# Optimization experiments

Measured on AMD Instinct MI355X. Metric: run time of the kernel, lower is better.

## Reference

```python
import jax, jax.numpy as jnp
import numpy as np

NG, NU, NI, H = 5000, 100000, 20000, 128
E_UG, E_UI, E_GI = 300000, 600000, 200000


def setup_inputs() -> dict:
    key = jax.random.key(0)
    ks = jax.random.split(key, 20)
    s = 0.05  # weight scale for numeric stability
    inp = {
        'x_group': jnp.arange(NG, dtype=jnp.int64) if False else jnp.arange(NG),
        'x_user': jnp.arange(NU),
        'x_item': jnp.arange(NI),
        'emb_group': jax.random.normal(ks[0], (NG, H), jnp.float32) * s,
        'emb_user': jax.random.normal(ks[1], (NU, H), jnp.float32) * s,
        'emb_item': jax.random.normal(ks[2], (NI, H), jnp.float32) * s,
        'W1l': jax.random.normal(ks[3], (6, H, H), jnp.float32) * s,
        'W1r': jax.random.normal(ks[4], (6, H, H), jnp.float32) * s,
        'b1': jax.random.normal(ks[5], (6, H), jnp.float32) * s,
        'W2l': jax.random.normal(ks[6], (6, H, H), jnp.float32) * s,
        'W2r': jax.random.normal(ks[7], (6, H, H), jnp.float32) * s,
        'b2': jax.random.normal(ks[8], (6, H), jnp.float32) * s,
        'pred_W': jax.random.normal(ks[9], (H, NI), jnp.float32) * s,
        'pred_b': jax.random.normal(ks[10], (NI,), jnp.float32) * s,
        'ug_src': jax.random.randint(ks[11], (E_UG,), 0, NU),
        'ug_dst': jax.random.randint(ks[12], (E_UG,), 0, NG),
        'ui_src': jax.random.randint(ks[13], (E_UI,), 0, NU),
        'ui_dst': jax.random.randint(ks[14], (E_UI,), 0, NI),
        'gi_src': jax.random.randint(ks[15], (E_GI,), 0, NG),
        'gi_dst': jax.random.randint(ks[16], (E_GI,), 0, NI),
    }
    return inp


def _seg_mean(x, src, dst, n_dst):
    # gather neighbor features [E, H], scatter-sum to dst, divide by in-degree
    s = jax.ops.segment_sum(x[src], dst, num_segments=n_dst)
    cnt = jax.ops.segment_sum(jnp.ones(dst.shape[0], x.dtype), dst, num_segments=n_dst)
    return s / jnp.clip(cnt, 1.0)[:, None]


def _hetero_sage_layer(hg, hu, hi, Wl, Wr, b,
                       ug_src, ug_dst, ui_src, ui_dst, gi_src, gi_dst):
    # edge-type order: 0 u2g, 1 g2u, 2 u2i, 3 i2u, 4 g2i, 5 i2g
    ng, nu, ni = hg.shape[0], hu.shape[0], hi.shape[0]
    og = (_seg_mean(hu, ug_src, ug_dst, ng) @ Wl[0] + hg @ Wr[0] + b[0]
          + _seg_mean(hi, gi_dst, gi_src, ng) @ Wl[5] + hg @ Wr[5] + b[5])
    ou = (_seg_mean(hg, ug_dst, ug_src, nu) @ Wl[1] + hu @ Wr[1] + b[1]
          + _seg_mean(hi, ui_dst, ui_src, nu) @ Wl[3] + hu @ Wr[3] + b[3])
    oi = (_seg_mean(hu, ui_src, ui_dst, ni) @ Wl[2] + hi @ Wr[2] + b[2]
          + _seg_mean(hg, gi_src, gi_dst, ni) @ Wl[4] + hi @ Wr[4] + b[4])
    return og, ou, oi


def reference(x_group, x_user, x_item, emb_group, emb_user, emb_item,
              W1l, W1r, b1, W2l, W2r, b2, pred_W, pred_b,
              ug_src, ug_dst, ui_src, ui_dst, gi_src, gi_dst):
    # embedding lookup; group embeddings are zeroed in BaseGR.forward
    hg = emb_group[x_group] * 0.0
    hu = emb_user[x_user]
    hi = emb_item[x_item]
    og, ou, oi = _hetero_sage_layer(hg, hu, hi, W1l, W1r, b1,
                                    ug_src, ug_dst, ui_src, ui_dst, gi_src, gi_dst)
    hg, hu, hi = jax.nn.relu(og), jax.nn.relu(ou), jax.nn.relu(oi)
    og, ou, oi = _hetero_sage_layer(hg, hu, hi, W2l, W2r, b2,
                                    ug_src, ug_dst, ui_src, ui_dst, gi_src, gi_dst)
    rep_group = jax.nn.relu(og)
    # eval-mode output: group-level item scores [NG, NI]
    return rep_group @ pred_W + pred_b
```

## Files before the change

kernel.cpp:

```cpp
#include <hip/hip_runtime.h>

typedef __bf16 bf16x8 __attribute__((ext_vector_type(8)));
typedef __bf16 bf16x4 __attribute__((ext_vector_type(4)));
typedef __bf16 bf16x2 __attribute__((ext_vector_type(2)));
typedef float  f32x4  __attribute__((ext_vector_type(4)));

#define NG 5000
#define NU 100000
#define NI 20000
#define H  128
#define EUG 300000
#define EUI 600000
#define EGI 200000
#define ETOT (EUG + EGI + EUI + EUI)
#define NN  (2 * NG + NU + NI)

#define B_EMBU  0UL
#define B_EMBI  25600000UL
#define B_AGGU  30720000UL
#define B_AGGI  56320000UL
#define B_AGGG1 61440000UL
#define B_AGGG2 62720000UL
#define B_HG1   64000000UL
#define B_GU    65280000UL
#define B_GI    66560000UL
#define B_REP   67840000UL
#define B_BC    69120000UL
#define B_PWT   69122048UL
#define B_WT    74242048UL
#define B_CNT   74536960UL
#define B_OFFS  75056960UL
#define B_CUR   75576976UL
#define B_EIDX  76096976UL



#define SCAN_CHUNK 2048
#define NCHUNK 64

__device__ __forceinline__ int swz(int row, int k) {
  return ((((k >> 3) ^ (row & 15)) << 3) | (k & 7));
}
__device__ __forceinline__ int cswz(int row, int col) {
  return col ^ (((row >> 2) & 1) << 4);
}

__global__ void prep_weights(const float* __restrict__ W1l, const float* __restrict__ W1r,
                             const float* __restrict__ W2l, const float* __restrict__ W2r,
                             const float* __restrict__ b1, const float* __restrict__ b2,
                             __bf16* __restrict__ WT, float* __restrict__ bc) {
  int b = blockIdx.x, tid = threadIdx.x;
  if (b < 9) {
    const float* Wa; const float* Wb = nullptr;
    switch (b) {
      case 0: Wa = W1r + 1 * 16384; Wb = W1r + 3 * 16384; break;
      case 1: Wa = W1l + 3 * 16384; break;
      case 2: Wa = W1l + 2 * 16384; break;
      case 3: Wa = W1r + 2 * 16384; Wb = W1r + 4 * 16384; break;
      case 4: Wa = W1l + 0 * 16384; break;
      case 5: Wa = W1l + 5 * 16384; break;
      case 6: Wa = W2r + 0 * 16384; Wb = W2r + 5 * 16384; break;
      case 7: Wa = W2l + 0 * 16384; break;
      default: Wa = W2l + 5 * 16384; break;
    }
    __bf16* dst = WT + b * 16384;
    for (int idx = tid; idx < 16384; idx += 256) {
      int k = idx >> 7, c = idx & 127;
      float v = Wa[idx];
      if (Wb) v += Wb[idx];
      dst[c * 128 + k] = (__bf16)v;
    }
  } else {
    if (tid < 128) {
      bc[tid]       = b1[128 + tid]     + b1[3 * 128 + tid];
      bc[128 + tid] = b1[2 * 128 + tid] + b1[4 * 128 + tid];
      bc[256 + tid] = b1[tid]           + b1[5 * 128 + tid];
      bc[384 + tid] = b2[tid]           + b2[5 * 128 + tid];
    }
  }
}

__global__ void transpose_predw(const float* __restrict__ pw, __bf16* __restrict__ pwt) {
  __shared__ float t[64][65];
  int i0 = blockIdx.x * 64, k0 = blockIdx.y * 64;
  int tid = threadIdx.x;
  for (int idx = tid; idx < 64 * 16; idx += 256) {
    int kk = idx >> 4, c4 = (idx & 15) << 2;
    int ib = i0 + c4;
    float x0 = 0.f, x1 = 0.f, x2 = 0.f, x3 = 0.f;
    const float* src = pw + (size_t)(k0 + kk) * NI + ib;
    if (ib + 3 < NI) {
      const float4 v = *(const float4*)src;
      x0 = v.x; x1 = v.y; x2 = v.z; x3 = v.w;
    } else {
      if (ib + 0 < NI) x0 = src[0];
      if (ib + 1 < NI) x1 = src[1];
      if (ib + 2 < NI) x2 = src[2];
      if (ib + 3 < NI) x3 = src[3];
    }
    t[kk][c4 + 0] = x0; t[kk][c4 + 1] = x1; t[kk][c4 + 2] = x2; t[kk][c4 + 3] = x3;
  }
  __syncthreads();
  for (int idx = tid; idx < 64 * 16; idx += 256) {
    int ii = idx >> 4, k4 = (idx & 15) << 2;
    int gi = i0 + ii;
    if (gi < NI) {
      bf16x4 o;
      o[0] = (__bf16)t[k4 + 0][ii]; o[1] = (__bf16)t[k4 + 1][ii];
      o[2] = (__bf16)t[k4 + 2][ii]; o[3] = (__bf16)t[k4 + 3][ii];
      *(bf16x4*)(pwt + (size_t)gi * 128 + k0 + k4) = o;
    }
  }
}

__global__ void cvt_bf16(const float* __restrict__ src, __bf16* __restrict__ dst, int n4) {
  int i = blockIdx.x * 256 + threadIdx.x;
  if (i < n4) {
    float4 v = ((const float4*)src)[i];
    bf16x4 o;
    o[0] = (__bf16)v.x; o[1] = (__bf16)v.y; o[2] = (__bf16)v.z; o[3] = (__bf16)v.w;
    ((bf16x4*)dst)[i] = o;
  }
}

__global__ void hist_all(const int* __restrict__ ug_dst, const int* __restrict__ gi_src,
                         const int* __restrict__ ui_src, const int* __restrict__ ui_dst,
                         int* __restrict__ cnt) {
  int i = blockIdx.x * 256 + threadIdx.x;
  int key, base;
  if (i < EUG)                       { key = ug_dst[i];                   base = 0; }
  else if (i < EUG + EGI)            { key = gi_src[i - EUG];             base = NG; }
  else if (i < EUG + EGI + EUI)      { key = ui_src[i - EUG - EGI];       base = 2 * NG; }
  else if (i < ETOT)                 { key = ui_dst[i - EUG - EGI - EUI]; base = 2 * NG + NU; }
  else return;
  atomicAdd(&cnt[base + key], 1);
}

__global__ void scan_k1(const int* __restrict__ cnt, int* __restrict__ chunksum) {
  __shared__ int ws[4];
  int b = blockIdx.x, tid = threadIdx.x, lane = tid & 63, w = tid >> 6;
  int base = b * SCAN_CHUNK + tid * 8;
  int s = 0;
#pragma unroll
  for (int j = 0; j < 8; ++j) { int i = base + j; if (i < NN) s += cnt[i]; }
#pragma unroll
  for (int d = 1; d < 64; d <<= 1) s += __shfl_xor(s, d, 64);
  if (lane == 0) ws[w] = s;
  __syncthreads();
  if (tid == 0) chunksum[b] = ws[0] + ws[1] + ws[2] + ws[3];
}

__global__ void scan_k2(const int* __restrict__ chunksum, int* __restrict__ chunkbase) {
  int lane = threadIdx.x;
  int v = chunksum[lane];
  int incl = v;
#pragma unroll
  for (int d = 1; d < 64; d <<= 1) { int t = __shfl_up(incl, d, 64); if (lane >= d) incl += t; }
  chunkbase[lane] = incl - v;
}

__global__ void scan_k3(const int* __restrict__ cnt, const int* __restrict__ chunkbase,
                        int* __restrict__ offs, int* __restrict__ cur) {
  __shared__ int ws[4];
  int b = blockIdx.x, tid = threadIdx.x, lane = tid & 63, w = tid >> 6;
  int base = b * SCAN_CHUNK + tid * 8;
  int x[8]; int s = 0;
#pragma unroll
  for (int j = 0; j < 8; ++j) { int i = base + j; x[j] = (i < NN) ? cnt[i] : 0; s += x[j]; }
  int incl = s;
#pragma unroll
  for (int d = 1; d < 64; d <<= 1) { int t = __shfl_up(incl, d, 64); if (lane >= d) incl += t; }
  if (lane == 63) ws[w] = incl;
  __syncthreads();
  int wpre = 0;
  for (int ww = 0; ww < w; ++ww) wpre += ws[ww];
  int excl = chunkbase[b] + wpre + incl - s;
#pragma unroll
  for (int j = 0; j < 8; ++j) {
    int i = base + j;
    if (i < NN) { offs[i] = excl; cur[i] = excl; }
    excl += x[j];
    if (i == NN - 1) offs[NN] = excl;
  }
}

__global__ void fill_all(const int* __restrict__ ug_src, const int* __restrict__ ug_dst,
                         const int* __restrict__ gi_src, const int* __restrict__ gi_dst,
                         const int* __restrict__ ui_src, const int* __restrict__ ui_dst,
                         int* __restrict__ cur, int* __restrict__ eidx) {
  int i = blockIdx.x * 256 + threadIdx.x;
  int key, base, payload;
  if (i < EUG)                  { key = ug_dst[i];       base = 0;            payload = ug_src[i]; }
  else if (i < EUG + EGI)       { int j = i - EUG;       key = gi_src[j]; base = NG;          payload = gi_dst[j]; }
  else if (i < EUG + EGI + EUI) { int j = i - EUG - EGI; key = ui_src[j]; base = 2 * NG;      payload = ui_dst[j]; }
  else if (i < ETOT)            { int j = i - EUG - EGI - EUI; key = ui_dst[j]; base = 2 * NG + NU; payload = ui_src[j]; }
  else return;
  int pos = atomicAdd(&cur[base + key], 1);
  eidx[pos] = payload;
}

__global__ __launch_bounds__(256)
void seg_mean_bf(const __bf16* __restrict__ feat, const int* __restrict__ offs,
                 const int* __restrict__ eidx, __bf16* __restrict__ out, int nnode) {
  int w = threadIdx.x >> 6, lane = threadIdx.x & 63;
  int node = blockIdx.x * 4 + w;
  if (node >= nnode) return;
  int s = offs[node], e = offs[node + 1];
  float a0 = 0.f, a1 = 0.f;
  int j = s;
  for (; j + 4 <= e; j += 4) {
    int i0 = eidx[j], i1 = eidx[j + 1], i2 = eidx[j + 2], i3 = eidx[j + 3];
    bf16x2 v0 = *(const bf16x2*)(feat + (size_t)i0 * 128 + lane * 2);
    bf16x2 v1 = *(const bf16x2*)(feat + (size_t)i1 * 128 + lane * 2);
    bf16x2 v2 = *(const bf16x2*)(feat + (size_t)i2 * 128 + lane * 2);
    bf16x2 v3 = *(const bf16x2*)(feat + (size_t)i3 * 128 + lane * 2);
    a0 += (float)v0[0] + (float)v1[0] + (float)v2[0] + (float)v3[0];
    a1 += (float)v0[1] + (float)v1[1] + (float)v2[1] + (float)v3[1];
  }
  for (; j < e; ++j) {
    int i0 = eidx[j];
    bf16x2 v0 = *(const bf16x2*)(feat + (size_t)i0 * 128 + lane * 2);
    a0 += (float)v0[0]; a1 += (float)v0[1];
  }
  float inv = (e > s) ? (1.f / (float)(e - s)) : 0.f;
  bf16x2 o;
  o[0] = (__bf16)(a0 * inv); o[1] = (__bf16)(a1 * inv);
  *(bf16x2*)(out + (size_t)node * 128 + lane * 2) = o;
}

__global__ __launch_bounds__(256)
void gemm_fused(const __bf16* __restrict__ A0, const __bf16* __restrict__ B0,
                const __bf16* __restrict__ A1, const __bf16* __restrict__ B1,
                const __bf16* __restrict__ A2, const __bf16* __restrict__ B2,
                const float* __restrict__ bias, float* __restrict__ Cf,
                __bf16* __restrict__ Cb, int N, int NC, int nterms, int relu) {
  __shared__ char smem_raw[128 * 128 * 4];
  __bf16* sA = (__bf16*)smem_raw;
  __bf16* sB = sA + 128 * 128;
  float* sC = (float*)smem_raw;
  int tid = threadIdx.x;
  int rowbase = blockIdx.x * 128, colbase = blockIdx.y * 128;
  int wid = tid >> 6, lane = tid & 63;
  int qrow = (wid >> 1) << 6, qcol = (wid & 1) << 6;
  int lrow = lane & 15, quad = lane >> 4;

  f32x4 acc[4][4];
#pragma unroll
  for (int mi = 0; mi < 4; ++mi)
#pragma unroll
    for (int ni = 0; ni < 4; ++ni) acc[mi][ni] = (f32x4){0.f, 0.f, 0.f, 0.f};

  const __bf16* As[3] = {A0, A1, A2};
  const __bf16* Bs[3] = {B0, B1, B2};

  for (int t = 0; t < nterms; ++t) {
    __syncthreads();
    const __bf16* A = As[t];
    for (int idx = tid; idx < 2048; idx += 256) {
      int row = idx >> 4, c8 = (idx & 15) << 3;
      int grow = rowbase + row;
      bf16x8 v;
      if (grow < N) v = *(const bf16x8*)(A + (size_t)grow * 128 + c8);
      else { for (int u = 0; u < 8; ++u) v[u] = (__bf16)0.f; }
      *(bf16x8*)&sA[row * 128 + swz(row, c8)] = v;
    }
    const __bf16* B = Bs[t];
    for (int idx = tid; idx < 2048; idx += 256) {
      int n = idx >> 4, c8 = (idx & 15) << 3;
      int gcol = colbase + n;
      bf16x8 v;
      if (gcol < NC) v = *(const bf16x8*)(B + (size_t)gcol * 128 + c8);
      else { for (int u = 0; u < 8; ++u) v[u] = (__bf16)0.f; }
      *(bf16x8*)&sB[n * 128 + swz(n, c8)] = v;
    }
    __syncthreads();
#pragma unroll
    for (int kb = 0; kb < 4; ++kb) {
      int k0 = kb * 32 + quad * 8;
      bf16x8 af[4], bfr[4];
#pragma unroll
      for (int mi = 0; mi < 4; ++mi) {
        int r = qrow + mi * 16 + lrow;
        af[mi] = *(const bf16x8*)&sA[r * 128 + swz(r, k0)];
      }
#pragma unroll
      for (int ni = 0; ni < 4; ++ni) {
        int r = qcol + ni * 16 + lrow;
        bfr[ni] = *(const bf16x8*)&sB[r * 128 + swz(r, k0)];
      }
#pragma unroll
      for (int mi = 0; mi < 4; ++mi)
#pragma unroll
        for (int ni = 0; ni < 4; ++ni)
          acc[mi][ni] = __builtin_amdgcn_mfma_f32_16x16x32_bf16(af[mi], bfr[ni], acc[mi][ni], 0, 0, 0);
    }
  }

  __syncthreads();
#pragma unroll
  for (int mi = 0; mi < 4; ++mi) {
#pragma unroll
    for (int ni = 0; ni < 4; ++ni) {
      int col = qcol + ni * 16 + lrow;
#pragma unroll
      for (int r = 0; r < 4; ++r) {
        int row = qrow + mi * 16 + quad * 4 + r;
        sC[row * 128 + cswz(row, col)] = acc[mi][ni][r];
      }
    }
  }
  __syncthreads();
  for (int idx = tid; idx < 4096; idx += 256) {
    int row = idx >> 5, c4 = (idx & 31) << 2;
    int grow = rowbase + row, gcol = colbase + c4;
    if (grow >= N) continue;
    f32x4 v = *(const f32x4*)&sC[row * 128 + cswz(row, c4)];
    if (gcol + 3 < NC) {
      f32x4 bv = *(const f32x4*)&bias[gcol];
      v += bv;
      if (relu) {
#pragma unroll
        for (int u = 0; u < 4; ++u) v[u] = fmaxf(v[u], 0.f);
      }
      if (Cb) {
        bf16x4 o;
        o[0] = (__bf16)v[0]; o[1] = (__bf16)v[1]; o[2] = (__bf16)v[2]; o[3] = (__bf16)v[3];
        *(bf16x4*)(Cb + (size_t)grow * NC + gcol) = o;
      } else {
        *(f32x4*)(Cf + (size_t)grow * NC + gcol) = v;
      }
    } else {
#pragma unroll
      for (int u = 0; u < 4; ++u) {
        if (gcol + u < NC) {
          float x = v[u] + bias[gcol + u];
          if (relu) x = fmaxf(x, 0.f);
          if (Cb) Cb[(size_t)grow * NC + gcol + u] = (__bf16)x;
          else    Cf[(size_t)grow * NC + gcol + u] = x;
        }
      }
    }
  }
}

extern "C" void kernel_launch(void* const* d_in, const int* in_sizes, int n_in,
                              void* d_out, int out_size, void* d_ws, size_t ws_size,
                              hipStream_t stream) {
  const float* emb_user = (const float*)d_in[4];
  const float* emb_item = (const float*)d_in[5];
  const float* W1l = (const float*)d_in[6];
  const float* W1r = (const float*)d_in[7];
  const float* b1  = (const float*)d_in[8];
  const float* W2l = (const float*)d_in[9];
  const float* W2r = (const float*)d_in[10];
  const float* b2  = (const float*)d_in[11];
  const float* predW = (const float*)d_in[12];
  const float* predb = (const float*)d_in[13];
  const int* ug_src = (const int*)d_in[14];
  const int* ug_dst = (const int*)d_in[15];
  const int* ui_src = (const int*)d_in[16];
  const int* ui_dst = (const int*)d_in[17];
  const int* gi_src = (const int*)d_in[18];
  const int* gi_dst = (const int*)d_in[19];

  char* ws = (char*)d_ws;
  __bf16* embU = (__bf16*)(ws + B_EMBU);
  __bf16* embI = (__bf16*)(ws + B_EMBI);
  __bf16* aggU = (__bf16*)(ws + B_AGGU);
  __bf16* aggI = (__bf16*)(ws + B_AGGI);
  __bf16* aggG1 = (__bf16*)(ws + B_AGGG1);
  __bf16* aggG2 = (__bf16*)(ws + B_AGGG2);
  __bf16* hg1 = (__bf16*)(ws + B_HG1);
  __bf16* gU  = (__bf16*)(ws + B_GU);
  __bf16* gI  = (__bf16*)(ws + B_GI);
  __bf16* rep = (__bf16*)(ws + B_REP);
  float* bc    = (float*)(ws + B_BC);
  __bf16* predWT = (__bf16*)(ws + B_PWT);
  __bf16* WT     = (__bf16*)(ws + B_WT);
  int* cnt  = (int*)(ws + B_CNT);
  int* offs = (int*)(ws + B_OFFS);
  int* cur  = (int*)(ws + B_CUR);
  int* eidx = (int*)(ws + B_EIDX);
  int* chunksum  = (int*)(ws + B_AGGU);
  int* chunkbase = chunksum + NCHUNK;

  const int* offs_ug  = offs;
  const int* offs_gi  = offs + NG;
  const int* offs_uiu = offs + 2 * NG;
  const int* offs_uii = offs + 2 * NG + NU;

  hipMemsetAsync(cnt, 0, NN * sizeof(int), stream);

  prep_weights<<<10, 256, 0, stream>>>(W1l, W1r, W2l, W2r, b1, b2, WT, bc);
  transpose_predw<<<dim3((NI + 63) / 64, 2), 256, 0, stream>>>(predW, predWT);
  cvt_bf16<<<(NU * 32 + 255) / 256, 256, 0, stream>>>(emb_user, embU, NU * 32);
  cvt_bf16<<<(NI * 32 + 255) / 256, 256, 0, stream>>>(emb_item, embI, NI * 32);

  hist_all<<<(ETOT + 255) / 256, 256, 0, stream>>>(ug_dst, gi_src, ui_src, ui_dst, cnt);
  scan_k1<<<NCHUNK, 256, 0, stream>>>(cnt, chunksum);
  scan_k2<<<1, 64, 0, stream>>>(chunksum, chunkbase);
  scan_k3<<<NCHUNK, 256, 0, stream>>>(cnt, chunkbase, offs, cur);
  fill_all<<<(ETOT + 255) / 256, 256, 0, stream>>>(ug_src, ug_dst, gi_src, gi_dst,
                                                   ui_src, ui_dst, cur, eidx);

  seg_mean_bf<<<(NU + 3) / 4, 256, 0, stream>>>(embI, offs_uiu, eidx, aggU, NU);
  seg_mean_bf<<<(NI + 3) / 4, 256, 0, stream>>>(embU, offs_uii, eidx, aggI, NI);
  seg_mean_bf<<<(NG + 3) / 4, 256, 0, stream>>>(embU, offs_ug, eidx, aggG1, NG);
  seg_mean_bf<<<(NG + 3) / 4, 256, 0, stream>>>(embI, offs_gi, eidx, aggG2, NG);

  gemm_fused<<<dim3((NU + 127) / 128, 1), 256, 0, stream>>>(
      embU, WT + 0 * 16384, aggU, WT + 1 * 16384, nullptr, nullptr,
      bc + 0, nullptr, aggU, NU, 128, 2, 1);
  gemm_fused<<<dim3((NI + 127) / 128, 1), 256, 0, stream>>>(
      aggI, WT + 2 * 16384, embI, WT + 3 * 16384, nullptr, nullptr,
      bc + 128, nullptr, aggI, NI, 128, 2, 1);
  gemm_fused<<<dim3((NG + 127) / 128, 1), 256, 0, stream>>>(
      aggG1, WT + 4 * 16384, aggG2, WT + 5 * 16384, nullptr, nullptr,
      bc + 256, nullptr, hg1, NG, 128, 2, 1);

  seg_mean_bf<<<(NG + 3) / 4, 256, 0, stream>>>(aggU, offs_ug, eidx, gU, NG);
  seg_mean_bf<<<(NG + 3) / 4, 256, 0, stream>>>(aggI, offs_gi, eidx, gI, NG);

  gemm_fused<<<dim3((NG + 127) / 128, 1), 256, 0, stream>>>(
      gU, WT + 7 * 16384, hg1, WT + 6 * 16384, gI, WT + 8 * 16384,
      bc + 384, nullptr, rep, NG, 128, 3, 1);

  gemm_fused<<<dim3((NG + 127) / 128, (NI + 127) / 128), 256, 0, stream>>>(
      rep, predWT, nullptr, nullptr, nullptr, nullptr,
      predb, (float*)d_out, nullptr, NG, NI, 1, 0);
}
```

Measured before the change: 1.043 ms.

## Fuse launches into phase kernels and pre-transform item embeddings before user aggregation

Several small launches are merged into combined kernels: prep, transpose, conversion and histogram run as one launch, the scan steps are merged, the four segment means run as one launch, and the layer-1 GEMMs run as one launch. By linearity, the item embeddings are multiplied by W1l[3] before the user-side mean, so aggU already holds the projected term and the user GEMM drops from two terms to one. That item GEMM runs alongside the scan blocks. The intent is to cut launch overhead and tail idle time and to remove one GEMM term over the large user set. The cost is an extra NI-row GEMM and a 5 MB buffer.

```diff
diff --git a/kernel.cpp b/kernel.cpp
--- a/kernel.cpp
+++ b/kernel.cpp
@@ -32,12 +32,23 @@
 #define B_OFFS  75056960UL
 #define B_CUR   75576976UL
 #define B_EIDX  76096976UL
-
+#define B_EIT   82897024UL
 
 
 #define SCAN_CHUNK 2048
 #define NCHUNK 64
 
+#define NB_PREP 10
+#define NB_TP   626
+#define NB_CVU  12500
+#define NB_CVI  2500
+#define NB_HIST 6641
+#define NB_P1   (NB_PREP + NB_TP + NB_CVU + NB_CVI + NB_HIST)
+
+#define NBU 782
+#define NBI 157
+#define NBG 40
+
 __device__ __forceinline__ int swz(int row, int k) {
   return ((((k >> 3) ^ (row & 15)) << 3) | (k & 7));
 }
@@ -45,11 +56,10 @@
   return col ^ (((row >> 2) & 1) << 4);
 }
 
-__global__ void prep_weights(const float* __restrict__ W1l, const float* __restrict__ W1r,
-                             const float* __restrict__ W2l, const float* __restrict__ W2r,
-                             const float* __restrict__ b1, const float* __restrict__ b2,
-                             __bf16* __restrict__ WT, float* __restrict__ bc) {
-  int b = blockIdx.x, tid = threadIdx.x;
+__device__ void prep_dev(const float* __restrict__ W1l, const float* __restrict__ W1r,
+                         const float* __restrict__ W2l, const float* __restrict__ W2r,
+                         const float* __restrict__ b1, const float* __restrict__ b2,
+                         __bf16* __restrict__ WT, float* __restrict__ bc, int b, int tid) {
   if (b < 9) {
     const float* Wa; const float* Wb = nullptr;
     switch (b) {
@@ -80,10 +90,9 @@
   }
 }
 
-__global__ void transpose_predw(const float* __restrict__ pw, __bf16* __restrict__ pwt) {
-  __shared__ float t[64][65];
-  int i0 = blockIdx.x * 64, k0 = blockIdx.y * 64;
-  int tid = threadIdx.x;
+__device__ void transpose_dev(const float* __restrict__ pw, __bf16* __restrict__ pwt,
+                              int bx, int by, int tid, float (*t)[65]) {
+  int i0 = bx * 64, k0 = by * 64;
   for (int idx = tid; idx < 64 * 16; idx += 256) {
     int kk = idx >> 4, c4 = (idx & 15) << 2;
     int ib = i0 + c4;
@@ -113,8 +122,9 @@
   }
 }
 
-__global__ void cvt_bf16(const float* __restrict__ src, __bf16* __restrict__ dst, int n4) {
-  int i = blockIdx.x * 256 + threadIdx.x;
+__device__ void cvt_dev(const float* __restrict__ src, __bf16* __restrict__ dst,
+                        int b, int tid, int n4) {
+  int i = b * 256 + tid;
   if (i < n4) {
     float4 v = ((const float4*)src)[i];
     bf16x4 o;
@@ -123,10 +133,10 @@
   }
 }
 
-__global__ void hist_all(const int* __restrict__ ug_dst, const int* __restrict__ gi_src,
+__device__ void hist_dev(const int* __restrict__ ug_dst, const int* __restrict__ gi_src,
                          const int* __restrict__ ui_src, const int* __restrict__ ui_dst,
-                         int* __restrict__ cnt) {
-  int i = blockIdx.x * 256 + threadIdx.x;
+                         int* __restrict__ cnt, int b, int tid) {
+  int i = b * 256 + tid;
   int key, base;
   if (i < EUG)                       { key = ug_dst[i];                   base = 0; }
   else if (i < EUG + EGI)            { key = gi_src[i - EUG];             base = NG; }
@@ -136,75 +146,132 @@
   atomicAdd(&cnt[base + key], 1);
 }
 
-__global__ void scan_k1(const int* __restrict__ cnt, int* __restrict__ chunksum) {
-  __shared__ int ws[4];
-  int b = blockIdx.x, tid = threadIdx.x, lane = tid & 63, w = tid >> 6;
-  int base = b * SCAN_CHUNK + tid * 8;
-  int s = 0;
-#pragma unroll
-  for (int j = 0; j < 8; ++j) { int i = base + j; if (i < NN) s += cnt[i]; }
-#pragma unroll
-  for (int d = 1; d < 64; d <<= 1) s += __shfl_xor(s, d, 64);
-  if (lane == 0) ws[w] = s;
+__device__ void gemm_core(const __bf16* __restrict__ A0, const __bf16* __restrict__ B0,
+                          const __bf16* __restrict__ A1, const __bf16* __restrict__ B1,
+                          const __bf16* __restrict__ A2, const __bf16* __restrict__ B2,
+                          const __bf16* __restrict__ Dadd, const float* __restrict__ bias,
+                          float* __restrict__ Cf, __bf16* __restrict__ Cb,
+                          int N, int NC, int nterms, int relu,
+                          int rowblk, int colblk, char* smem_raw) {
+  __bf16* sA = (__bf16*)smem_raw;
+  __bf16* sB = sA + 128 * 128;
+  float* sC = (float*)smem_raw;
+  int tid = threadIdx.x;
+  int rowbase = rowblk * 128, colbase = colblk * 128;
+  int wid = tid >> 6, lane = tid & 63;
+  int qrow = (wid >> 1) << 6, qcol = (wid & 1) << 6;
+  int lrow = lane & 15, quad = lane >> 4;
+
+  f32x4 acc[4][4];
+#pragma unroll
+  for (int mi = 0; mi < 4; ++mi)
+#pragma unroll
+    for (int ni = 0; ni < 4; ++ni) acc[mi][ni] = (f32x4){0.f, 0.f, 0.f, 0.f};
+
+  const __bf16* As[3] = {A0, A1, A2};
+  const __bf16* Bs[3] = {B0, B1, B2};
+
+  for (int t = 0; t < nterms; ++t) {
+    __syncthreads();
+    const __bf16* A = As[t];
+    for (int idx = tid; idx < 2048; idx += 256) {
+      int row = idx >> 4, c8 = (idx & 15) << 3;
+      int grow = rowbase + row;
+      bf16x8 v;
+      if (grow < N) v = *(const bf16x8*)(A + (size_t)grow * 128 + c8);
+      else { for (int u = 0; u < 8; ++u) v[u] = (__bf16)0.f; }
+      *(bf16x8*)&sA[row * 128 + swz(row, c8)] = v;
+    }
+    const __bf16* B = Bs[t];
+    for (int idx = tid; idx < 2048; idx += 256) {
+      int n = idx >> 4, c8 = (idx & 15) << 3;
+      int gcol = colbase + n;
+      bf16x8 v;
+      if (gcol < NC) v = *(const bf16x8*)(B + (size_t)gcol * 128 + c8);
+      else { for (int u = 0; u < 8; ++u) v[u] = (__bf16)0.f; }
+      *(bf16x8*)&sB[n * 128 + swz(n, c8)] = v;
+    }
+    __syncthreads();
+#pragma unroll
+    for (int kb = 0; kb < 4; ++kb) {
+      int k0 = kb * 32 + quad * 8;
+      bf16x8 af[4], bfr[4];
+#pragma unroll
+      for (int mi = 0; mi < 4; ++mi) {
+        int r = qrow + mi * 16 + lrow;
+        af[mi] = *(const bf16x8*)&sA[r * 128 + swz(r, k0)];
+      }
+#pragma unroll
+      for (int ni = 0; ni < 4; ++ni) {
+        int r = qcol + ni * 16 + lrow;
+        bfr[ni] = *(const bf16x8*)&sB[r * 128 + swz(r, k0)];
+      }
+#pragma unroll
+      for (int mi = 0; mi < 4; ++mi)
+#pragma unroll
+        for (int ni = 0; ni < 4; ++ni)
+          acc[mi][ni] = __builtin_amdgcn_mfma_f32_16x16x32_bf16(af[mi], bfr[ni], acc[mi][ni], 0, 0, 0);
+    }
+  }
+
   __syncthreads();
-  if (tid == 0) chunksum[b] = ws[0] + ws[1] + ws[2] + ws[3];
-}
-
-__global__ void scan_k2(const int* __restrict__ chunksum, int* __restrict__ chunkbase) {
-  int lane = threadIdx.x;
-  int v = chunksum[lane];
-  int incl = v;
-#pragma unroll
-  for (int d = 1; d < 64; d <<= 1) { int t = __shfl_up(incl, d, 64); if (lane >= d) incl += t; }
-  chunkbase[lane] = incl - v;
-}
-
-__global__ void scan_k3(const int* __restrict__ cnt, const int* __restrict__ chunkbase,
-                        int* __restrict__ offs, int* __restrict__ cur) {
-  __shared__ int ws[4];
-  int b = blockIdx.x, tid = threadIdx.x, lane = tid & 63, w = tid >> 6;
-  int base = b * SCAN_CHUNK + tid * 8;
-  int x[8]; int s = 0;
-#pragma unroll
-  for (int j = 0; j < 8; ++j) { int i = base + j; x[j] = (i < NN) ? cnt[i] : 0; s += x[j]; }
-  int incl = s;
-#pragma unroll
-  for (int d = 1; d < 64; d <<= 1) { int t = __shfl_up(incl, d, 64); if (lane >= d) incl += t; }
-  if (lane == 63) ws[w] = incl;
+#pragma unroll
+  for (int mi = 0; mi < 4; ++mi) {
+#pragma unroll
+    for (int ni = 0; ni < 4; ++ni) {
+      int col = qcol + ni * 16 + lrow;
+#pragma unroll
+      for (int r = 0; r < 4; ++r) {
+        int row = qrow + mi * 16 + quad * 4 + r;
+        sC[row * 128 + cswz(row, col)] = acc[mi][ni][r];
+      }
+    }
+  }
   __syncthreads();
-  int wpre = 0;
-  for (int ww = 0; ww < w; ++ww) wpre += ws[ww];
-  int excl = chunkbase[b] + wpre + incl - s;
-#pragma unroll
-  for (int j = 0; j < 8; ++j) {
-    int i = base + j;
-    if (i < NN) { offs[i] = excl; cur[i] = excl; }
-    excl += x[j];
-    if (i == NN - 1) offs[NN] = excl;
-  }
-}
-
-__global__ void fill_all(const int* __restrict__ ug_src, const int* __restrict__ ug_dst,
-                         const int* __restrict__ gi_src, const int* __restrict__ gi_dst,
-                         const int* __restrict__ ui_src, const int* __restrict__ ui_dst,
-                         int* __restrict__ cur, int* __restrict__ eidx) {
-  int i = blockIdx.x * 256 + threadIdx.x;
-  int key, base, payload;
-  if (i < EUG)                  { key = ug_dst[i];       base = 0;            payload = ug_src[i]; }
-  else if (i < EUG + EGI)       { int j = i - EUG;       key = gi_src[j]; base = NG;          payload = gi_dst[j]; }
-  else if (i < EUG + EGI + EUI) { int j = i - EUG - EGI; key = ui_src[j]; base = 2 * NG;      payload = ui_dst[j]; }
-  else if (i < ETOT)            { int j = i - EUG - EGI - EUI; key = ui_dst[j]; base = 2 * NG + NU; payload = ui_src[j]; }
-  else return;
-  int pos = atomicAdd(&cur[base + key], 1);
-  eidx[pos] = payload;
-}
-
-__global__ __launch_bounds__(256)
-void seg_mean_bf(const __bf16* __restrict__ feat, const int* __restrict__ offs,
-                 const int* __restrict__ eidx, __bf16* __restrict__ out, int nnode) {
-  int w = threadIdx.x >> 6, lane = threadIdx.x & 63;
-  int node = blockIdx.x * 4 + w;
-  if (node >= nnode) return;
+  for (int idx = tid; idx < 4096; idx += 256) {
+    int row = idx >> 5, c4 = (idx & 31) << 2;
+    int grow = rowbase + row, gcol = colbase + c4;
+    if (grow >= N) continue;
+    f32x4 v = *(const f32x4*)&sC[row * 128 + cswz(row, c4)];
+    if (gcol + 3 < NC) {
+      if (bias) {
+        f32x4 bv = *(const f32x4*)&bias[gcol];
+        v += bv;
+      }
+      if (Dadd) {
+        bf16x4 dv = *(const bf16x4*)(Dadd + (size_t)grow * 128 + gcol);
+        v[0] += (float)dv[0]; v[1] += (float)dv[1];
+        v[2] += (float)dv[2]; v[3] += (float)dv[3];
+      }
+      if (relu) {
+#pragma unroll
+        for (int u = 0; u < 4; ++u) v[u] = fmaxf(v[u], 0.f);
+      }
+      if (Cb) {
+        bf16x4 o;
+        o[0] = (__bf16)v[0]; o[1] = (__bf16)v[1]; o[2] = (__bf16)v[2]; o[3] = (__bf16)v[3];
+        *(bf16x4*)(Cb + (size_t)grow * NC + gcol) = o;
+      } else {
+        __builtin_nontemporal_store(v, (f32x4*)(Cf + (size_t)grow * NC + gcol));
+      }
+    } else {
+#pragma unroll
+      for (int u = 0; u < 4; ++u) {
+        if (gcol + u < NC) {
+          float x = v[u] + (bias ? bias[gcol + u] : 0.f);
+          if (Dadd) x += (float)Dadd[(size_t)grow * 128 + gcol + u];
+          if (relu) x = fmaxf(x, 0.f);
+          if (Cb) Cb[(size_t)grow * NC + gcol + u] = (__bf16)x;
+          else    Cf[(size_t)grow * NC + gcol + u] = x;
+        }
+      }
+    }
+  }
+}
+
+__device__ void seg_dev(const __bf16* __restrict__ feat, const int* __restrict__ offs,
+                        const int* __restrict__ eidx, __bf16* __restrict__ out,
+                        int node, int orow, int lane) {
   int s = offs[node], e = offs[node + 1];
   float a0 = 0.f, a1 = 0.f;
   int j = s;
@@ -217,7 +284,15 @@
     a0 += (float)v0[0] + (float)v1[0] + (float)v2[0] + (float)v3[0];
     a1 += (float)v0[1] + (float)v1[1] + (float)v2[1] + (float)v3[1];
   }
-  for (; j < e; ++j) {
+  if (j + 2 <= e) {
+    int i0 = eidx[j], i1 = eidx[j + 1];
+    bf16x2 v0 = *(const bf16x2*)(feat + (size_t)i0 * 128 + lane * 2);
+    bf16x2 v1 = *(const bf16x2*)(feat + (size_t)i1 * 128 + lane * 2);
+    a0 += (float)v0[0] + (float)v1[0];
+    a1 += (float)v0[1] + (float)v1[1];
+    j += 2;
+  }
+  if (j < e) {
     int i0 = eidx[j];
     bf16x2 v0 = *(const bf16x2*)(feat + (size_t)i0 * 128 + lane * 2);
     a0 += (float)v0[0]; a1 += (float)v0[1];
@@ -225,122 +300,185 @@
   float inv = (e > s) ? (1.f / (float)(e - s)) : 0.f;
   bf16x2 o;
   o[0] = (__bf16)(a0 * inv); o[1] = (__bf16)(a1 * inv);
-  *(bf16x2*)(out + (size_t)node * 128 + lane * 2) = o;
-}
-
-__global__ __launch_bounds__(256)
-void gemm_fused(const __bf16* __restrict__ A0, const __bf16* __restrict__ B0,
-                const __bf16* __restrict__ A1, const __bf16* __restrict__ B1,
-                const __bf16* __restrict__ A2, const __bf16* __restrict__ B2,
-                const float* __restrict__ bias, float* __restrict__ Cf,
-                __bf16* __restrict__ Cb, int N, int NC, int nterms, int relu) {
-  __shared__ char smem_raw[128 * 128 * 4];
-  __bf16* sA = (__bf16*)smem_raw;
-  __bf16* sB = sA + 128 * 128;
-  float* sC = (float*)smem_raw;
-  int tid = threadIdx.x;
-  int rowbase = blockIdx.x * 128, colbase = blockIdx.y * 128;
-  int wid = tid >> 6, lane = tid & 63;
-  int qrow = (wid >> 1) << 6, qcol = (wid & 1) << 6;
-  int lrow = lane & 15, quad = lane >> 4;
-
-  f32x4 acc[4][4];
-#pragma unroll
-  for (int mi = 0; mi < 4; ++mi)
-#pragma unroll
-    for (int ni = 0; ni < 4; ++ni) acc[mi][ni] = (f32x4){0.f, 0.f, 0.f, 0.f};
-
-  const __bf16* As[3] = {A0, A1, A2};
-  const __bf16* Bs[3] = {B0, B1, B2};
-
-  for (int t = 0; t < nterms; ++t) {
+  *(bf16x2*)(out + (size_t)orow * 128 + lane * 2) = o;
+}
+
+__global__ __launch_bounds__(256)
+void phase1(const float* __restrict__ W1l, const float* __restrict__ W1r,
+            const float* __restrict__ W2l, const float* __restrict__ W2r,
+            const float* __restrict__ b1, const float* __restrict__ b2,
+            const float* __restrict__ predW,
+            const float* __restrict__ emb_user, const float* __restrict__ emb_item,
+            const int* __restrict__ ug_dst, const int* __restrict__ gi_src,
+            const int* __restrict__ ui_src, const int* __restrict__ ui_dst,
+            char* __restrict__ ws) {
+  __shared__ float tbuf[64][65];
+  __bf16* WT = (__bf16*)(ws + B_WT);
+  float* bc  = (float*)(ws + B_BC);
+  __bf16* pwt = (__bf16*)(ws + B_PWT);
+  __bf16* embU = (__bf16*)(ws + B_EMBU);
+  __bf16* embI = (__bf16*)(ws + B_EMBI);
+  int* cnt = (int*)(ws + B_CNT);
+  int b = blockIdx.x, tid = threadIdx.x;
+  if (b < NB_PREP) { prep_dev(W1l, W1r, W2l, W2r, b1, b2, WT, bc, b, tid); return; }
+  b -= NB_PREP;
+  if (b < NB_TP) { transpose_dev(predW, pwt, b % 313, b / 313, tid, tbuf); return; }
+  b -= NB_TP;
+  if (b < NB_CVU) { cvt_dev(emb_user, embU, b, tid, NU * 32); return; }
+  b -= NB_CVU;
+  if (b < NB_CVI) { cvt_dev(emb_item, embI, b, tid, NI * 32); return; }
+  b -= NB_CVI;
+  hist_dev(ug_dst, gi_src, ui_src, ui_dst, cnt, b, tid);
+}
+
+__global__ __launch_bounds__(256)
+void scan_k1(const int* __restrict__ cnt, int* __restrict__ chunksum) {
+  __shared__ int ws4[4];
+  int b = blockIdx.x, tid = threadIdx.x, lane = tid & 63, w = tid >> 6;
+  int base = b * SCAN_CHUNK + tid * 8;
+  int s = 0;
+#pragma unroll
+  for (int j = 0; j < 8; ++j) { int i = base + j; if (i < NN) s += cnt[i]; }
+#pragma unroll
+  for (int d = 1; d < 64; d <<= 1) s += __shfl_xor(s, d, 64);
+  if (lane == 0) ws4[w] = s;
+  __syncthreads();
+  if (tid == 0) chunksum[b] = ws4[0] + ws4[1] + ws4[2] + ws4[3];
+}
+
+__global__ __launch_bounds__(256)
+void scan2_gemm0(char* __restrict__ ws) {
+  __shared__ char smem[65536];
+  int b = blockIdx.x, tid = threadIdx.x;
+  if (b < NCHUNK) {
+    int* shi = (int*)smem;
+    const int* cnt = (const int*)(ws + B_CNT);
+    const int* chunksum = (const int*)(ws + B_AGGU);
+    int* offs = (int*)(ws + B_OFFS);
+    int* cur  = (int*)(ws + B_CUR);
+    int lane = tid & 63, w = tid >> 6;
+    if (w == 0) {
+      int v = chunksum[lane];
+      int incl = v;
+#pragma unroll
+      for (int d = 1; d < 64; d <<= 1) { int t = __shfl_up(incl, d, 64); if (lane >= d) incl += t; }
+      if (lane == b) shi[4] = incl - v;
+    }
+    int base = b * SCAN_CHUNK + tid * 8;
+    int x[8]; int s = 0;
+#pragma unroll
+    for (int j = 0; j < 8; ++j) { int i = base + j; x[j] = (i < NN) ? cnt[i] : 0; s += x[j]; }
+    int incl = s;
+#pragma unroll
+    for (int d = 1; d < 64; d <<= 1) { int t = __shfl_up(incl, d, 64); if (lane >= d) incl += t; }
+    if (lane == 63) shi[w] = incl;
     __syncthreads();
-    const __bf16* A = As[t];
-    for (int idx = tid; idx < 2048; idx += 256) {
-      int row = idx >> 4, c8 = (idx & 15) << 3;
-      int grow = rowbase + row;
-      bf16x8 v;
-      if (grow < N) v = *(const bf16x8*)(A + (size_t)grow * 128 + c8);
-      else { for (int u = 0; u < 8; ++u) v[u] = (__bf16)0.f; }
-      *(bf16x8*)&sA[row * 128 + swz(row, c8)] = v;
-    }
-    const __bf16* B = Bs[t];
-    for (int idx = tid; idx < 2048; idx += 256) {
-      int n = idx >> 4, c8 = (idx & 15) << 3;
-      int gcol = colbase + n;
-      bf16x8 v;
-      if (gcol < NC) v = *(const bf16x8*)(B + (size_t)gcol * 128 + c8);
-      else { for (int u = 0; u < 8; ++u) v[u] = (__bf16)0.f; }
-      *(bf16x8*)&sB[n * 128 + swz(n, c8)] = v;
-    }
-    __syncthreads();
-#pragma unroll
-    for (int kb = 0; kb < 4; ++kb) {
-      int k0 = kb * 32 + quad * 8;
-      bf16x8 af[4], bfr[4];
-#pragma unroll
-      for (int mi = 0; mi < 4; ++mi) {
-        int r = qrow + mi * 16 + lrow;
-        af[mi] = *(const bf16x8*)&sA[r * 128 + swz(r, k0)];
-      }
-#pragma unroll
-      for (int ni = 0; ni < 4; ++ni) {
-        int r = qcol + ni * 16 + lrow;
-        bfr[ni] = *(const bf16x8*)&sB[r * 128 + swz(r, k0)];
-      }
-#pragma unroll
-      for (int mi = 0; mi < 4; ++mi)
-#pragma unroll
-        for (int ni = 0; ni < 4; ++ni)
-          acc[mi][ni] = __builtin_amdgcn_mfma_f32_16x16x32_bf16(af[mi], bfr[ni], acc[mi][ni], 0, 0, 0);
-    }
-  }
-
-  __syncthreads();
-#pragma unroll
-  for (int mi = 0; mi < 4; ++mi) {
-#pragma unroll
-    for (int ni = 0; ni < 4; ++ni) {
-      int col = qcol + ni * 16 + lrow;
-#pragma unroll
-      for (int r = 0; r < 4; ++r) {
-        int row = qrow + mi * 16 + quad * 4 + r;
-        sC[row * 128 + cswz(row, col)] = acc[mi][ni][r];
-      }
-    }
-  }
-  __syncthreads();
-  for (int idx = tid; idx < 4096; idx += 256) {
-    int row = idx >> 5, c4 = (idx & 31) << 2;
-    int grow = rowbase + row, gcol = colbase + c4;
-    if (grow >= N) continue;
-    f32x4 v = *(const f32x4*)&sC[row * 128 + cswz(row, c4)];
-    if (gcol + 3 < NC) {
-      f32x4 bv = *(const f32x4*)&bias[gcol];
-      v += bv;
-      if (relu) {
-#pragma unroll
-        for (int u = 0; u < 4; ++u) v[u] = fmaxf(v[u], 0.f);
-      }
-      if (Cb) {
-        bf16x4 o;
-        o[0] = (__bf16)v[0]; o[1] = (__bf16)v[1]; o[2] = (__bf16)v[2]; o[3] = (__bf16)v[3];
-        *(bf16x4*)(Cb + (size_t)grow * NC + gcol) = o;
-      } else {
-        *(f32x4*)(Cf + (size_t)grow * NC + gcol) = v;
-      }
-    } else {
-#pragma unroll
-      for (int u = 0; u < 4; ++u) {
-        if (gcol + u < NC) {
-          float x = v[u] + bias[gcol + u];
-          if (relu) x = fmaxf(x, 0.f);
-          if (Cb) Cb[(size_t)grow * NC + gcol + u] = (__bf16)x;
-          else    Cf[(size_t)grow * NC + gcol + u] = x;
-        }
-      }
-    }
-  }
+    int wpre = 0;
+    for (int ww = 0; ww < w; ++ww) wpre += shi[ww];
+    int excl = shi[4] + wpre + incl - s;
+#pragma unroll
+    for (int j = 0; j < 8; ++j) {
+      int i = base + j;
+      if (i < NN) { offs[i] = excl; cur[i] = excl; }
+      excl += x[j];
+      if (i == NN - 1) offs[NN] = excl;
+    }
+  } else {
+    const __bf16* embI = (const __bf16*)(ws + B_EMBI);
+    const __bf16* WT   = (const __bf16*)(ws + B_WT);
+    __bf16* eit = (__bf16*)(ws + B_EIT);
+    gemm_core(embI, WT + 1 * 16384, nullptr, nullptr, nullptr, nullptr,
+              nullptr, nullptr, nullptr, eit, NI, 128, 1, 0, b - NCHUNK, 0, smem);
+  }
+}
+
+__global__ __launch_bounds__(256)
+void fill_all(const int* __restrict__ ug_src, const int* __restrict__ ug_dst,
+              const int* __restrict__ gi_src, const int* __restrict__ gi_dst,
+              const int* __restrict__ ui_src, const int* __restrict__ ui_dst,
+              int* __restrict__ cur, int* __restrict__ eidx) {
+  int i = blockIdx.x * 256 + threadIdx.x;
+  int key, base, payload;
+  if (i < EUG)                  { key = ug_dst[i];       base = 0;            payload = ug_src[i]; }
+  else if (i < EUG + EGI)       { int j = i - EUG;       key = gi_src[j]; base = NG;          payload = gi_dst[j]; }
+  else if (i < EUG + EGI + EUI) { int j = i - EUG - EGI; key = ui_src[j]; base = 2 * NG;      payload = ui_dst[j]; }
+  else if (i < ETOT)            { int j = i - EUG - EGI - EUI; key = ui_dst[j]; base = 2 * NG + NU; payload = ui_src[j]; }
+  else return;
+  int pos = atomicAdd(&cur[base + key], 1);
+  eidx[pos] = payload;
+}
+
+__global__ __launch_bounds__(256)
+void seg1(char* __restrict__ ws) {
+  int w = threadIdx.x >> 6, lane = threadIdx.x & 63;
+  int node = blockIdx.x * 4 + w;
+  if (node >= NN) return;
+  const int* offs = (const int*)(ws + B_OFFS);
+  const int* eidx = (const int*)(ws + B_EIDX);
+  const __bf16* feat; __bf16* out; int orow;
+  if (node < NG)               { feat = (const __bf16*)(ws + B_EMBU); out = (__bf16*)(ws + B_AGGG1); orow = node; }
+  else if (node < 2 * NG)      { feat = (const __bf16*)(ws + B_EMBI); out = (__bf16*)(ws + B_AGGG2); orow = node - NG; }
+  else if (node < 2 * NG + NU) { feat = (const __bf16*)(ws + B_EIT);  out = (__bf16*)(ws + B_AGGU);  orow = node - 2 * NG; }
+  else                         { feat = (const __bf16*)(ws + B_EMBU); out = (__bf16*)(ws + B_AGGI);  orow = node - 2 * NG - NU; }
+  seg_dev(feat, offs, eidx, out, node, orow, lane);
+}
+
+__global__ __launch_bounds__(256)
+void gemm1(char* __restrict__ ws) {
+  __shared__ char smem[65536];
+  const __bf16* WT = (const __bf16*)(ws + B_WT);
+  const float* bc  = (const float*)(ws + B_BC);
+  int b = blockIdx.x;
+  if (b < NBU) {
+    __bf16* aggU = (__bf16*)(ws + B_AGGU);
+    gemm_core((const __bf16*)(ws + B_EMBU), WT + 0 * 16384,
+              nullptr, nullptr, nullptr, nullptr,
+              aggU, bc + 0, nullptr, aggU, NU, 128, 1, 1, b, 0, smem);
+  } else if (b < NBU + NBI) {
+    __bf16* aggI = (__bf16*)(ws + B_AGGI);
+    gemm_core(aggI, WT + 2 * 16384,
+              (const __bf16*)(ws + B_EMBI), WT + 3 * 16384, nullptr, nullptr,
+              nullptr, bc + 128, nullptr, aggI, NI, 128, 2, 1, b - NBU, 0, smem);
+  } else {
+    gemm_core((const __bf16*)(ws + B_AGGG1), WT + 4 * 16384,
+              (const __bf16*)(ws + B_AGGG2), WT + 5 * 16384, nullptr, nullptr,
+              nullptr, bc + 256, nullptr, (__bf16*)(ws + B_HG1), NG, 128, 2, 1,
+              b - NBU - NBI, 0, smem);
+  }
+}
+
+__global__ __launch_bounds__(256)
+void seg2(char* __restrict__ ws) {
+  int w = threadIdx.x >> 6, lane = threadIdx.x & 63;
+  int node = blockIdx.x * 4 + w;
+  if (node >= 2 * NG) return;
+  const int* offs = (const int*)(ws + B_OFFS);
+  const int* eidx = (const int*)(ws + B_EIDX);
+  const __bf16* feat; __bf16* out; int orow;
+  if (node < NG) { feat = (const __bf16*)(ws + B_AGGU); out = (__bf16*)(ws + B_GU); orow = node; }
+  else           { feat = (const __bf16*)(ws + B_AGGI); out = (__bf16*)(ws + B_GI); orow = node - NG; }
+  seg_dev(feat, offs, eidx, out, node, orow, lane);
+}
+
+__global__ __launch_bounds__(256)
+void gemm2(char* __restrict__ ws) {
+  __shared__ char smem[65536];
+  const __bf16* WT = (const __bf16*)(ws + B_WT);
+  const float* bc  = (const float*)(ws + B_BC);
+  gemm_core((const __bf16*)(ws + B_GU),  WT + 7 * 16384,
+            (const __bf16*)(ws + B_HG1), WT + 6 * 16384,
+            (const __bf16*)(ws + B_GI),  WT + 8 * 16384,
+            nullptr, bc + 384, nullptr, (__bf16*)(ws + B_REP), NG, 128, 3, 1,
+            blockIdx.x, 0, smem);
+}
+
+__global__ __launch_bounds__(256)
+void gemmF(char* __restrict__ ws, const float* __restrict__ predb, float* __restrict__ out) {
+  __shared__ char smem[65536];
+  gemm_core((const __bf16*)(ws + B_REP), (const __bf16*)(ws + B_PWT),
+            nullptr, nullptr, nullptr, nullptr,
+            nullptr, predb, out, nullptr, NG, NI, 1, 0,
+            blockIdx.x, blockIdx.y, smem);
 }
 
 extern "C" void kernel_launch(void* const* d_in, const int* in_sizes, int n_in,
@@ -364,68 +502,23 @@
   const int* gi_dst = (const int*)d_in[19];
 
   char* ws = (char*)d_ws;
-  __bf16* embU = (__bf16*)(ws + B_EMBU);
-  __bf16* embI = (__bf16*)(ws + B_EMBI);
-  __bf16* aggU = (__bf16*)(ws + B_AGGU);
-  __bf16* aggI = (__bf16*)(ws + B_AGGI);
-  __bf16* aggG1 = (__bf16*)(ws + B_AGGG1);
-  __bf16* aggG2 = (__bf16*)(ws + B_AGGG2);
-  __bf16* hg1 = (__bf16*)(ws + B_HG1);
-  __bf16* gU  = (__bf16*)(ws + B_GU);
-  __bf16* gI  = (__bf16*)(ws + B_GI);
-  __bf16* rep = (__bf16*)(ws + B_REP);
-  float* bc    = (float*)(ws + B_BC);
-  __bf16* predWT = (__bf16*)(ws + B_PWT);
-  __bf16* WT     = (__bf16*)(ws + B_WT);
   int* cnt  = (int*)(ws + B_CNT);
-  int* offs = (int*)(ws + B_OFFS);
   int* cur  = (int*)(ws + B_CUR);
   int* eidx = (int*)(ws + B_EIDX);
-  int* chunksum  = (int*)(ws + B_AGGU);
-  int* chunkbase = chunksum + NCHUNK;
-
-  const int* offs_ug  = offs;
-  const int* offs_gi  = offs + NG;
-  const int* offs_uiu = offs + 2 * NG;
-  const int* offs_uii = offs + 2 * NG + NU;
+  int* chunksum = (int*)(ws + B_AGGU);
 
   hipMemsetAsync(cnt, 0, NN * sizeof(int), stream);
 
-  prep_weights<<<10, 256, 0, stream>>>(W1l, W1r, W2l, W2r, b1, b2, WT, bc);
-  transpose_predw<<<dim3((NI + 63) / 64, 2), 256, 0, stream>>>(predW, predWT);
-  cvt_bf16<<<(NU * 32 + 255) / 256, 256, 0, stream>>>(emb_user, embU, NU * 32);
-  cvt_bf16<<<(NI * 32 + 255) / 256, 256, 0, stream>>>(emb_item, embI, NI * 32);
-
-  hist_all<<<(ETOT + 255) / 256, 256, 0, stream>>>(ug_dst, gi_src, ui_src, ui_dst, cnt);
+  phase1<<<NB_P1, 256, 0, stream>>>(W1l, W1r, W2l, W2r, b1, b2, predW,
+                                    emb_user, emb_item,
+                                    ug_dst, gi_src, ui_src, ui_dst, ws);
   scan_k1<<<NCHUNK, 256, 0, stream>>>(cnt, chunksum);
-  scan_k2<<<1, 64, 0, stream>>>(chunksum, chunkbase);
-  scan_k3<<<NCHUNK, 256, 0, stream>>>(cnt, chunkbase, offs, cur);
+  scan2_gemm0<<<NCHUNK + NBI, 256, 0, stream>>>(ws);
   fill_all<<<(ETOT + 255) / 256, 256, 0, stream>>>(ug_src, ug_dst, gi_src, gi_dst,
                                                    ui_src, ui_dst, cur, eidx);
-
-  seg_mean_bf<<<(NU + 3) / 4, 256, 0, stream>>>(embI, offs_uiu, eidx, aggU, NU);
-  seg_mean_bf<<<(NI + 3) / 4, 256, 0, stream>>>(embU, offs_uii, eidx, aggI, NI);
-  seg_mean_bf<<<(NG + 3) / 4, 256, 0, stream>>>(embU, offs_ug, eidx, aggG1, NG);
-  seg_mean_bf<<<(NG + 3) / 4, 256, 0, stream>>>(embI, offs_gi, eidx, aggG2, NG);
-
-  gemm_fused<<<dim3((NU + 127) / 128, 1), 256, 0, stream>>>(
-      embU, WT + 0 * 16384, aggU, WT + 1 * 16384, nullptr, nullptr,
-      bc + 0, nullptr, aggU, NU, 128, 2, 1);
-  gemm_fused<<<dim3((NI + 127) / 128, 1), 256, 0, stream>>>(
-      aggI, WT + 2 * 16384, embI, WT + 3 * 16384, nullptr, nullptr,
-      bc + 128, nullptr, aggI, NI, 128, 2, 1);
-  gemm_fused<<<dim3((NG + 127) / 128, 1), 256, 0, stream>>>(
-      aggG1, WT + 4 * 16384, aggG2, WT + 5 * 16384, nullptr, nullptr,
-      bc + 256, nullptr, hg1, NG, 128, 2, 1);
-
-  seg_mean_bf<<<(NG + 3) / 4, 256, 0, stream>>>(aggU, offs_ug, eidx, gU, NG);
-  seg_mean_bf<<<(NG + 3) / 4, 256, 0, stream>>>(aggI, offs_gi, eidx, gI, NG);
-
-  gemm_fused<<<dim3((NG + 127) / 128, 1), 256, 0, stream>>>(
-      gU, WT + 7 * 16384, hg1, WT + 6 * 16384, gI, WT + 8 * 16384,
-      bc + 384, nullptr, rep, NG, 128, 3, 1);
-
-  gemm_fused<<<dim3((NG + 127) / 128, (NI + 127) / 128), 256, 0, stream>>>(
-      rep, predWT, nullptr, nullptr, nullptr, nullptr,
-      predb, (float*)d_out, nullptr, NG, NI, 1, 0);
-}
+  seg1<<<(NN + 3) / 4, 256, 0, stream>>>(ws);
+  gemm1<<<NBU + NBI + NBG, 256, 0, stream>>>(ws);
+  seg2<<<(2 * NG + 3) / 4, 256, 0, stream>>>(ws);
+  gemm2<<<NBG, 256, 0, stream>>>(ws);
+  gemmF<<<dim3(NBG, NBI), 256, 0, stream>>>(ws, predb, (float*)d_out);
+}
```

After: 924.5 us. -11.4%, faster.
